# Optimization experiments

Hardware: AMD Instinct MI355X
Metric: run time of the kernel (lower is better)

Reference implementation:

```python
import jax, jax.numpy as jnp
import numpy as np

TAU = 2.0          # LIF membrane time constant (spikingjelly default)
V_TH = 1.0         # v_threshold
V_RESET = 0.0      # hard reset value
ATAN_ALPHA = 2.0   # surrogate.ATan default alpha
EPS = 1e-12        # F.normalize eps

@jax.custom_vjp
def spike_fn(x):
    # Heaviside forward, ATan surrogate backward
    return (x >= 0).astype(x.dtype)

def _spike_fwd(x):
    return spike_fn(x), x

def _spike_bwd(x, g):
    sg = (ATAN_ALPHA / 2.0) / (1.0 + (jnp.pi / 2.0 * ATAN_ALPHA * x) ** 2)
    return (g * sg,)

spike_fn.defvjp(_spike_fwd, _spike_bwd)

def setup_inputs() -> dict:
    key = jax.random.key(0)
    k1, k2 = jax.random.split(key)
    T, B, F, H = 32, 512, 2048, 2048
    x_seq = jax.random.normal(k1, (T, B, F), dtype=jnp.float32)
    lim = float(np.sqrt(6.0 / (F + H)))  # xavier_uniform
    W = jax.random.uniform(k2, (H, F), dtype=jnp.float32, minval=-lim, maxval=lim)
    b = jnp.zeros((H,), dtype=jnp.float32)
    return {"x_seq": x_seq, "W": W, "b": b}

def reference(x_seq, W, b):
    # Linear: [T,B,F] @ [F,H] -> [T,B,H]
    cur = jnp.einsum('tbf,hf->tbh', x_seq, W) + b
    # F.normalize(dim=-1): L2 normalize the injected current per neuron vector
    norm = jnp.maximum(jnp.sqrt(jnp.sum(cur * cur, axis=-1, keepdims=True)), EPS)
    cur = cur / norm

    def step(v, c):
        # LIF charge: v <- v + (x - (v - v_reset)) / tau
        v = v + (c - (v - V_RESET)) / TAU
        s = spike_fn(v - V_TH)
        sd = jax.lax.stop_gradient(s)  # detach_reset=True
        v = v * (1.0 - sd) + V_RESET * sd  # hard reset
        return v, s

    v0 = jnp.zeros(cur.shape[1:], dtype=cur.dtype)  # [B,H]
    _, spk_seq = jax.lax.scan(step, v0, cur)  # spk_seq: [T,B,H]
    count = spk_seq.sum(axis=0)  # [B,H]
    return spk_seq, count
```

## Files before the change

kernel.cpp:

```cpp
#include <hip/hip_runtime.h>
#include <hip/hip_bf16.h>

#define T_SZ 32
#define B_SZ 512
#define F_SZ 2048
#define H_SZ 2048
#define M_SZ (T_SZ * B_SZ)

typedef short bf16x8 __attribute__((ext_vector_type(8)));
typedef float f32x4  __attribute__((ext_vector_type(4)));
typedef unsigned short u16x8 __attribute__((ext_vector_type(8)));

__device__ __forceinline__ void gload_lds16(const void* g, void* l) {
    __builtin_amdgcn_global_load_lds(
        (const __attribute__((address_space(1))) unsigned int*)g,
        (__attribute__((address_space(3))) unsigned int*)l,
        16, 0, 0);
}

__device__ __forceinline__ float bf16_bits_to_f32(unsigned short u) {
    return __uint_as_float(((unsigned)u) << 16);
}

__global__ __launch_bounds__(256) void cvt_bf16_kernel(const float* __restrict__ in,
                                                       unsigned short* __restrict__ out,
                                                       int n4) {
    int i = blockIdx.x * 256 + threadIdx.x;
    if (i >= n4) return;
    float4 v = ((const float4*)in)[i];
    ushort4 o;
    o.x = __builtin_bit_cast(unsigned short, __float2bfloat16(v.x));
    o.y = __builtin_bit_cast(unsigned short, __float2bfloat16(v.y));
    o.z = __builtin_bit_cast(unsigned short, __float2bfloat16(v.z));
    o.w = __builtin_bit_cast(unsigned short, __float2bfloat16(v.w));
    ((ushort4*)out)[i] = o;
}

__global__ __launch_bounds__(256) void gemm_bt_kernel(const __hip_bfloat16* __restrict__ A,
                                                      const __hip_bfloat16* __restrict__ Bt,
                                                      const float* __restrict__ bias,
                                                      __hip_bfloat16* __restrict__ C)
{
    __shared__ __align__(16) __hip_bfloat16 As[128 * 32];
    __shared__ __align__(16) __hip_bfloat16 Bs[128 * 32];

    const int tid  = threadIdx.x;
    const int lane = tid & 63;
    const int wave = tid >> 6;
    const int wm   = wave >> 1;
    const int wn   = wave & 1;
    const int m0   = blockIdx.y * 128;
    const int n0   = blockIdx.x * 128;
    const int quad = lane >> 4;
    const int r16  = lane & 15;

    f32x4 acc[4][4] = {};

    for (int k0 = 0; k0 < F_SZ; k0 += 32) {
        __syncthreads();
        #pragma unroll
        for (int j = 0; j < 2; ++j) {
            int chunk = j * 256 + tid;
            int row   = chunk >> 2;
            int kp    = (chunk & 3) << 3;
            gload_lds16(A  + (size_t)(m0 + row) * F_SZ + k0 + kp, (void*)(As + chunk * 8));
            gload_lds16(Bt + (size_t)(n0 + row) * F_SZ + k0 + kp, (void*)(Bs + chunk * 8));
        }
        __syncthreads();

        bf16x8 af[4], bq[4];
        #pragma unroll
        for (int i = 0; i < 4; ++i) {
            af[i] = *(const bf16x8*)(As + (wm * 64 + i * 16 + r16) * 32 + quad * 8);
            bq[i] = *(const bf16x8*)(Bs + (wn * 64 + i * 16 + r16) * 32 + quad * 8);
        }
        #pragma unroll
        for (int mi = 0; mi < 4; ++mi)
            #pragma unroll
            for (int ni = 0; ni < 4; ++ni)
                acc[mi][ni] = __builtin_amdgcn_mfma_f32_16x16x32_bf16(af[mi], bq[ni], acc[mi][ni], 0, 0, 0);
    }

    #pragma unroll
    for (int ni = 0; ni < 4; ++ni) {
        const int gn = n0 + wn * 64 + ni * 16 + r16;
        const float bv = bias[gn];
        #pragma unroll
        for (int mi = 0; mi < 4; ++mi) {
            const int gm = m0 + wm * 64 + mi * 16 + quad * 4;
            #pragma unroll
            for (int r = 0; r < 4; ++r)
                C[(size_t)(gm + r) * H_SZ + gn] = __float2bfloat16(acc[mi][ni][r] + bv);
        }
    }
}

__global__ __launch_bounds__(256) void row_ss_kernel(const __hip_bfloat16* __restrict__ cur,
                                                     float* __restrict__ ninv) {
    const int lane = threadIdx.x & 63;
    const int row  = blockIdx.x * 4 + (threadIdx.x >> 6);
    const __hip_bfloat16* rp = cur + (size_t)row * H_SZ;

    float s = 0.f;
    #pragma unroll
    for (int i = 0; i < 4; ++i) {
        const u16x8 pk = *(const u16x8*)(rp + i * 512 + lane * 8);
        #pragma unroll
        for (int j = 0; j < 8; ++j) {
            float f = bf16_bits_to_f32(pk[j]);
            s += f * f;
        }
    }
    #pragma unroll
    for (int off = 32; off >= 1; off >>= 1) s += __shfl_down(s, off, 64);
    if (lane == 0) ninv[row] = 1.0f / fmaxf(sqrtf(s), 1e-12f);
}

__global__ __launch_bounds__(256) void lif_scan_kernel(const __hip_bfloat16* __restrict__ cur,
                                                       const float* __restrict__ ninv,
                                                       float* __restrict__ spk,
                                                       float* __restrict__ cnt)
{
    const int gid = blockIdx.x * 256 + threadIdx.x;
    const int b   = gid >> 9;
    const int h0  = (gid & 511) * 4;

    float v[4]  = {0, 0, 0, 0};
    float cn[4] = {0, 0, 0, 0};
    #pragma unroll
    for (int t = 0; t < T_SZ; ++t) {
        const size_t off = (size_t)(t * B_SZ + b) * H_SZ + h0;
        const ushort4 pk = *(const ushort4*)(cur + off);
        const float inv  = ninv[t * B_SZ + b];
        float so[4];
        {
            float c;
            c = bf16_bits_to_f32(pk.x) * inv; v[0] += (c - v[0]) * 0.5f;
            c = bf16_bits_to_f32(pk.y) * inv; v[1] += (c - v[1]) * 0.5f;
            c = bf16_bits_to_f32(pk.z) * inv; v[2] += (c - v[2]) * 0.5f;
            c = bf16_bits_to_f32(pk.w) * inv; v[3] += (c - v[3]) * 0.5f;
        }
        #pragma unroll
        for (int j = 0; j < 4; ++j) {
            float s = (v[j] >= 1.0f) ? 1.0f : 0.0f;
            so[j] = s;
            cn[j] += s;
            v[j] = (s != 0.f) ? 0.f : v[j];
        }
        *(float4*)(spk + off) = make_float4(so[0], so[1], so[2], so[3]);
    }
    *(float4*)(cnt + (size_t)b * H_SZ + h0) = make_float4(cn[0], cn[1], cn[2], cn[3]);
}

extern "C" void kernel_launch(void* const* d_in, const int* in_sizes, int n_in,
                              void* d_out, int out_size, void* d_ws, size_t ws_size,
                              hipStream_t stream) {
    const float* x    = (const float*)d_in[0];
    const float* W    = (const float*)d_in[1];
    const float* bias = (const float*)d_in[2];

    float* spk = (float*)d_out;
    float* cnt = spk + (size_t)T_SZ * B_SZ * H_SZ;

    char* ws = (char*)d_ws;
    __hip_bfloat16* xb   = (__hip_bfloat16*)ws;
    __hip_bfloat16* Wb   = (__hip_bfloat16*)(ws + (size_t)M_SZ * F_SZ * 2);
    __hip_bfloat16* curb = (__hip_bfloat16*)(ws + (size_t)M_SZ * F_SZ * 2
                                                + (size_t)H_SZ * F_SZ * 2);
    float* ninv          = (float*)(ws + (size_t)M_SZ * F_SZ * 2
                                       + (size_t)H_SZ * F_SZ * 2
                                       + (size_t)M_SZ * H_SZ * 2);

    cvt_bf16_kernel<<<(M_SZ * F_SZ) / 1024, 256, 0, stream>>>(x, (unsigned short*)xb, (M_SZ * F_SZ) / 4);
    cvt_bf16_kernel<<<(H_SZ * F_SZ) / 1024, 256, 0, stream>>>(W, (unsigned short*)Wb, (H_SZ * F_SZ) / 4);
    gemm_bt_kernel<<<dim3(H_SZ / 128, M_SZ / 128), 256, 0, stream>>>(xb, Wb, bias, curb);
    row_ss_kernel<<<M_SZ / 4, 256, 0, stream>>>(curb, ninv);
    lif_scan_kernel<<<(B_SZ * H_SZ / 4) / 256, 256, 0, stream>>>(curb, ninv, spk, cnt);
}
```

Measured before the change: 430.5 us.

## Switch GEMM to FP8 inputs with 32x32x64 scaled MFMA and swizzled LDS

Converts x and W to FP8 (e4m3, with W pre-scaled by 256) instead of bf16, and replaces the bf16 16x16x32 MFMA GEMM with the gfx950 scaled f8f6f4 32x32x64 MFMA. It uses 64-wide K tiles with an XOR-swizzled LDS layout to avoid bank conflicts. This halves conversion write traffic and GEMM operand bytes and doubles MFMA throughput. The risk is much lower precision in the injected current, which could flip spikes near the threshold.

```diff
diff --git a/kernel.cpp b/kernel.cpp
--- a/kernel.cpp
+++ b/kernel.cpp
@@ -7,8 +7,8 @@
 #define H_SZ 2048
 #define M_SZ (T_SZ * B_SZ)
 
-typedef short bf16x8 __attribute__((ext_vector_type(8)));
-typedef float f32x4  __attribute__((ext_vector_type(4)));
+typedef int   i32x8  __attribute__((ext_vector_type(8)));
+typedef float f32x16 __attribute__((ext_vector_type(16)));
 typedef unsigned short u16x8 __attribute__((ext_vector_type(8)));
 
 __device__ __forceinline__ void gload_lds16(const void* g, void* l) {
@@ -22,27 +22,27 @@
     return __uint_as_float(((unsigned)u) << 16);
 }
 
-__global__ __launch_bounds__(256) void cvt_bf16_kernel(const float* __restrict__ in,
-                                                       unsigned short* __restrict__ out,
-                                                       int n4) {
+__global__ __launch_bounds__(256) void cvt_fp8_kernel(const float* __restrict__ in,
+                                                      unsigned int* __restrict__ out,
+                                                      float scale, int n8) {
     int i = blockIdx.x * 256 + threadIdx.x;
-    if (i >= n4) return;
-    float4 v = ((const float4*)in)[i];
-    ushort4 o;
-    o.x = __builtin_bit_cast(unsigned short, __float2bfloat16(v.x));
-    o.y = __builtin_bit_cast(unsigned short, __float2bfloat16(v.y));
-    o.z = __builtin_bit_cast(unsigned short, __float2bfloat16(v.z));
-    o.w = __builtin_bit_cast(unsigned short, __float2bfloat16(v.w));
-    ((ushort4*)out)[i] = o;
+    if (i >= n8) return;
+    float4 v0 = ((const float4*)in)[2 * i];
+    float4 v1 = ((const float4*)in)[2 * i + 1];
+    int w0 = __builtin_amdgcn_cvt_pk_fp8_f32(v0.x * scale, v0.y * scale, 0, false);
+    w0     = __builtin_amdgcn_cvt_pk_fp8_f32(v0.z * scale, v0.w * scale, w0, true);
+    int w1 = __builtin_amdgcn_cvt_pk_fp8_f32(v1.x * scale, v1.y * scale, 0, false);
+    w1     = __builtin_amdgcn_cvt_pk_fp8_f32(v1.z * scale, v1.w * scale, w1, true);
+    ((uint2*)out)[i] = make_uint2((unsigned)w0, (unsigned)w1);
 }
 
-__global__ __launch_bounds__(256) void gemm_bt_kernel(const __hip_bfloat16* __restrict__ A,
-                                                      const __hip_bfloat16* __restrict__ Bt,
-                                                      const float* __restrict__ bias,
-                                                      __hip_bfloat16* __restrict__ C)
+__global__ __launch_bounds__(256) void gemm_fp8_kernel(const unsigned char* __restrict__ A,
+                                                       const unsigned char* __restrict__ Bt,
+                                                       const float* __restrict__ bias,
+                                                       __hip_bfloat16* __restrict__ C)
 {
-    __shared__ __align__(16) __hip_bfloat16 As[128 * 32];
-    __shared__ __align__(16) __hip_bfloat16 Bs[128 * 32];
+    __shared__ __align__(16) unsigned char As[128 * 64];
+    __shared__ __align__(16) unsigned char Bs[128 * 64];
 
     const int tid  = threadIdx.x;
     const int lane = tid & 63;
@@ -51,46 +51,58 @@
     const int wn   = wave & 1;
     const int m0   = blockIdx.y * 128;
     const int n0   = blockIdx.x * 128;
-    const int quad = lane >> 4;
-    const int r16  = lane & 15;
+    const int l31  = lane & 31;
+    const int kh   = lane >> 5;
 
-    f32x4 acc[4][4] = {};
+    f32x16 acc[2][2] = {};
 
-    for (int k0 = 0; k0 < F_SZ; k0 += 32) {
+    for (int k0 = 0; k0 < F_SZ; k0 += 64) {
         __syncthreads();
         #pragma unroll
         for (int j = 0; j < 2; ++j) {
-            int chunk = j * 256 + tid;
-            int row   = chunk >> 2;
-            int kp    = (chunk & 3) << 3;
-            gload_lds16(A  + (size_t)(m0 + row) * F_SZ + k0 + kp, (void*)(As + chunk * 8));
-            gload_lds16(Bt + (size_t)(n0 + row) * F_SZ + k0 + kp, (void*)(Bs + chunk * 8));
+            int c   = j * 256 + tid;
+            int row = c >> 2;
+            int u   = (c & 3) ^ ((row >> 1) & 3);
+            gload_lds16(A  + (size_t)(m0 + row) * F_SZ + k0 + u * 16, (void*)(As + c * 16));
+            gload_lds16(Bt + (size_t)(n0 + row) * F_SZ + k0 + u * 16, (void*)(Bs + c * 16));
         }
         __syncthreads();
 
-        bf16x8 af[4], bq[4];
+        i32x8 af[2], bq[2];
         #pragma unroll
-        for (int i = 0; i < 4; ++i) {
-            af[i] = *(const bf16x8*)(As + (wm * 64 + i * 16 + r16) * 32 + quad * 8);
-            bq[i] = *(const bf16x8*)(Bs + (wn * 64 + i * 16 + r16) * 32 + quad * 8);
+        for (int i = 0; i < 2; ++i) {
+            const int ra = wm * 64 + i * 32 + l31;
+            const int rb = wn * 64 + i * 32 + l31;
+            const int sa = (ra >> 1) & 3;
+            const int sb = (rb >> 1) & 3;
+            ((int4*)&af[i])[0] = *(const int4*)(As + ra * 64 + (((kh * 2 + 0) ^ sa) * 16));
+            ((int4*)&af[i])[1] = *(const int4*)(As + ra * 64 + (((kh * 2 + 1) ^ sa) * 16));
+            ((int4*)&bq[i])[0] = *(const int4*)(Bs + rb * 64 + (((kh * 2 + 0) ^ sb) * 16));
+            ((int4*)&bq[i])[1] = *(const int4*)(Bs + rb * 64 + (((kh * 2 + 1) ^ sb) * 16));
         }
         #pragma unroll
-        for (int mi = 0; mi < 4; ++mi)
+        for (int mi = 0; mi < 2; ++mi)
             #pragma unroll
-            for (int ni = 0; ni < 4; ++ni)
-                acc[mi][ni] = __builtin_amdgcn_mfma_f32_16x16x32_bf16(af[mi], bq[ni], acc[mi][ni], 0, 0, 0);
+            for (int ni = 0; ni < 2; ++ni)
+                acc[mi][ni] = __builtin_amdgcn_mfma_scale_f32_32x32x64_f8f6f4(
+                    af[mi], bq[ni], acc[mi][ni],
+                    0 , 0 ,
+                    0, 0x7f7f7f7f,
+                    0, 0x7f7f7f7f);
     }
 
     #pragma unroll
-    for (int ni = 0; ni < 4; ++ni) {
-        const int gn = n0 + wn * 64 + ni * 16 + r16;
+    for (int ni = 0; ni < 2; ++ni) {
+        const int gn = n0 + wn * 64 + ni * 32 + l31;
         const float bv = bias[gn];
         #pragma unroll
-        for (int mi = 0; mi < 4; ++mi) {
-            const int gm = m0 + wm * 64 + mi * 16 + quad * 4;
+        for (int mi = 0; mi < 2; ++mi) {
+            const int gmb = m0 + wm * 64 + mi * 32 + 4 * kh;
             #pragma unroll
-            for (int r = 0; r < 4; ++r)
-                C[(size_t)(gm + r) * H_SZ + gn] = __float2bfloat16(acc[mi][ni][r] + bv);
+            for (int r = 0; r < 16; ++r) {
+                const int grow = gmb + (r & 3) + 8 * (r >> 2);
+                C[(size_t)grow * H_SZ + gn] = __float2bfloat16(acc[mi][ni][r] * (1.0f / 256.0f) + bv);
+            }
         }
     }
 }
@@ -163,17 +175,14 @@
     float* cnt = spk + (size_t)T_SZ * B_SZ * H_SZ;
 
     char* ws = (char*)d_ws;
-    __hip_bfloat16* xb   = (__hip_bfloat16*)ws;
-    __hip_bfloat16* Wb   = (__hip_bfloat16*)(ws + (size_t)M_SZ * F_SZ * 2);
-    __hip_bfloat16* curb = (__hip_bfloat16*)(ws + (size_t)M_SZ * F_SZ * 2
-                                                + (size_t)H_SZ * F_SZ * 2);
-    float* ninv          = (float*)(ws + (size_t)M_SZ * F_SZ * 2
-                                       + (size_t)H_SZ * F_SZ * 2
-                                       + (size_t)M_SZ * H_SZ * 2);
+    unsigned char* x8    = (unsigned char*)ws;
+    unsigned char* W8    = x8 + (size_t)M_SZ * F_SZ;
+    __hip_bfloat16* curb = (__hip_bfloat16*)(W8 + (size_t)H_SZ * F_SZ);
+    float* ninv          = (float*)((char*)curb + (size_t)M_SZ * H_SZ * 2);
 
-    cvt_bf16_kernel<<<(M_SZ * F_SZ) / 1024, 256, 0, stream>>>(x, (unsigned short*)xb, (M_SZ * F_SZ) / 4);
-    cvt_bf16_kernel<<<(H_SZ * F_SZ) / 1024, 256, 0, stream>>>(W, (unsigned short*)Wb, (H_SZ * F_SZ) / 4);
-    gemm_bt_kernel<<<dim3(H_SZ / 128, M_SZ / 128), 256, 0, stream>>>(xb, Wb, bias, curb);
+    cvt_fp8_kernel<<<(M_SZ * F_SZ / 8) / 256, 256, 0, stream>>>(x, (unsigned int*)x8, 1.0f,   M_SZ * F_SZ / 8);
+    cvt_fp8_kernel<<<(H_SZ * F_SZ / 8) / 256, 256, 0, stream>>>(W, (unsigned int*)W8, 256.0f, H_SZ * F_SZ / 8);
+    gemm_fp8_kernel<<<dim3(H_SZ / 128, M_SZ / 128), 256, 0, stream>>>(x8, W8, bias, curb);
     row_ss_kernel<<<M_SZ / 4, 256, 0, stream>>>(curb, ninv);
     lif_scan_kernel<<<(B_SZ * H_SZ / 4) / 256, 256, 0, stream>>>(curb, ninv, spk, cnt);
 }
```

Result: faster. 356.9 us (-17.1%).
